# Kernel optimization log

Hardware: AMD Instinct MI355X
Metric: run time of the kernel (lower is better)

The kernel has to match this reference:

```python
import jax, jax.numpy as jnp
import numpy as np

N = 100000        # nodes
E = 3200000       # edges
IN = 256          # in_feats
H = 8             # num_heads
O = 64            # out_feats
F = 64            # edge_feats
T = 8             # num_etypes

def setup_inputs() -> dict:
    key = jax.random.key(0)
    ks = jax.random.split(key, 10)
    return {
        "feat": jax.random.normal(ks[0], (N, IN), jnp.float32) * 0.1,
        "etype": jax.random.randint(ks[1], (E,), 0, T, jnp.int32),
        "src": jax.random.randint(ks[2], (E,), 0, N, jnp.int32),
        "dst": jax.random.randint(ks[3], (E,), 0, N, jnp.int32),
        "W_fc": jax.random.normal(ks[4], (IN, H * O), jnp.float32) * (1.0 / np.sqrt(IN)),
        "edge_emb": jax.random.normal(ks[5], (T, F), jnp.float32),
        "W_e": jax.random.normal(ks[6], (F, H * F), jnp.float32) * (1.0 / np.sqrt(F)),
        "attn_l": jax.random.normal(ks[7], (H, O), jnp.float32) * 0.1,
        "attn_r": jax.random.normal(ks[8], (H, O), jnp.float32) * 0.1,
        "attn_e": jax.random.normal(ks[9], (H, F), jnp.float32) * 0.1,
    }

def reference(feat, etype, src, dst, W_fc, edge_emb, W_e, attn_l, attn_r, attn_e):
    n = feat.shape[0]
    # node projection + per-head attention logits
    h = (feat @ W_fc).reshape(n, H, O)                      # [N,H,O]
    el = jnp.einsum('nho,ho->nh', h, attn_l)                # [N,H]
    er = jnp.einsum('nho,ho->nh', h, attn_r)                # [N,H]
    # edge-type embedding -> projection -> logit (project the tiny table once, then gather)
    emb_proj = (edge_emb @ W_e).reshape(T, H, F)            # [T,H,F]
    ee = jnp.einsum('thf,hf->th', emb_proj, attn_e)[etype]  # [E,H]
    # u_add_v + edge bias, then ReLU (module's "leaky_relu" is nn.ReLU())
    e = jax.nn.relu(el[src] + er[dst] + ee)                 # [E,H]
    # segment softmax grouped by destination node
    m = jax.ops.segment_max(e, dst, num_segments=n)         # [N,H]
    ex = jnp.exp(e - m[dst])                                # [E,H]
    s = jax.ops.segment_sum(ex, dst, num_segments=n)        # [N,H]
    return ex / s[dst]                                      # [E,H]
```

## Files before the change

### kernel.cpp

```cpp
#include <hip/hip_runtime.h>
#include <math.h>

#define NN 100000
#define NE 3200000
#define INF_ 256
#define NH 8
#define OF 64
#define EF 64
#define NT 8

#define BSH 7
#define BNODES 128
#define NB 782
#define CAPB 4608
#define SPLIT 2
#define CHUNK 2304
#define EPB 4096

static constexpr size_t WS_AT      = 0;
static constexpr size_t WS_EE      = 4096;
static constexpr size_t WS_EL      = 4160;
static constexpr size_t WS_ERS     = WS_EL + (size_t)NN * 8;
static constexpr size_t WS_CCNT    = WS_ERS + (size_t)NN * 16;
static constexpr size_t WS_PART    = WS_CCNT + NB + 2;
static constexpr size_t WS_PARTIAL = WS_PART + (size_t)NB * CAPB;

__global__ __launch_bounds__(256) void k_prep_A(const float* __restrict__ W_fc,
                                                const float* __restrict__ attn_l,
                                                const float* __restrict__ attn_r,
                                                float* __restrict__ At,
                                                unsigned* __restrict__ ccnt) {
    int t = blockIdx.x * 256 + threadIdx.x;
    if (t < NB) ccnt[t] = 0u;
    int c = t >> 8;
    int i = t & 255;
    int h = c & 7;
    const float* attn = (c < 8) ? attn_l : attn_r;
    const float* wrow = W_fc + (size_t)i * (NH * OF) + h * OF;
    const float* arow = attn + h * OF;
    float acc = 0.f;
#pragma unroll 8
    for (int o = 0; o < OF; ++o) acc += wrow[o] * arow[o];
    At[c * INF_ + i] = acc;
}

__global__ __launch_bounds__(512) void k_prep_ee(const float* __restrict__ edge_emb,
                                                 const float* __restrict__ W_e,
                                                 const float* __restrict__ attn_e,
                                                 float* __restrict__ ee_tab) {
    __shared__ float B[EF][NH];
    int t = threadIdx.x;
    int g = t >> 3, h = t & 7;
    const float* wrow = W_e + (size_t)g * (NH * EF) + h * EF;
    const float* arow = attn_e + h * EF;
    float acc = 0.f;
#pragma unroll 8
    for (int f = 0; f < EF; ++f) acc += wrow[f] * arow[f];
    B[g][h] = acc;
    __syncthreads();
    if (t < NT * NH) {
        int tt = t >> 3, hh = t & 7;
        float a = 0.f;
#pragma unroll 8
        for (int g2 = 0; g2 < EF; ++g2) a += edge_emb[tt * EF + g2] * B[g2][hh];
        ee_tab[tt * NH + hh] = a;
    }
}

__global__ __launch_bounds__(256) void k_node(const float* __restrict__ feat,
                                              const float* __restrict__ At,
                                              float* __restrict__ el,
                                              float* __restrict__ ers) {
    int n = blockIdx.x * 256 + threadIdx.x;
    if (n >= NN) return;
    const float4* f4 = (const float4*)(feat + (size_t)n * INF_);
    const float4* A4 = (const float4*)At;
    float acc[16];
#pragma unroll
    for (int c = 0; c < 16; ++c) acc[c] = 0.f;
    for (int iq = 0; iq < INF_ / 4; ++iq) {
        float4 f = f4[iq];
#pragma unroll
        for (int c = 0; c < 16; ++c) {
            float4 a = A4[c * 64 + iq];
            acc[c] += f.x * a.x + f.y * a.y + f.z * a.z + f.w * a.w;
        }
    }
    float4* e4 = (float4*)(el + (size_t)n * 8);
    e4[0] = make_float4(acc[0], acc[1], acc[2], acc[3]);
    e4[1] = make_float4(acc[4], acc[5], acc[6], acc[7]);
    float4* r4 = (float4*)(ers + (size_t)n * 16);
    r4[0] = make_float4(acc[8], acc[9], acc[10], acc[11]);
    r4[1] = make_float4(acc[12], acc[13], acc[14], acc[15]);
}

__global__ __launch_bounds__(256) void k_partition(const int* __restrict__ src,
                                                   const int* __restrict__ dst,
                                                   const int* __restrict__ etype,
                                                   unsigned* __restrict__ ccnt,
                                                   unsigned* __restrict__ part) {
    __shared__ unsigned hist[NB];
    __shared__ unsigned cursor[NB];
    int tid = threadIdx.x;
    size_t base = (size_t)blockIdx.x * EPB;
    unsigned long long rc[16];
    for (int i = tid; i < NB; i += 256) hist[i] = 0u;
    __syncthreads();
#pragma unroll
    for (int k = 0; k < 16; ++k) {
        size_t j = base + (size_t)k * 256 + tid;
        if (j < NE) {
            int dj = dst[j];
            rc[k] = (unsigned long long)(unsigned)src[j]
                  | ((unsigned long long)(unsigned)etype[j] << 17)
                  | ((unsigned long long)(unsigned)dj << 20);
            atomicAdd(&hist[dj >> BSH], 1u);
        } else rc[k] = ~0ull;
    }
    __syncthreads();
    for (int i = tid; i < NB; i += 256) {
        unsigned h = hist[i];
        cursor[i] = h ? atomicAdd(ccnt + i, h) : 0u;
    }
    __syncthreads();
#pragma unroll
    for (int k = 0; k < 16; ++k) {
        if (rc[k] == ~0ull) continue;
        int dj = (int)(rc[k] >> 20);
        int b = dj >> BSH;
        unsigned pos = atomicAdd(&cursor[b], 1u);
        if (pos < CAPB)
            part[(size_t)b * CAPB + pos] =
                (unsigned)(rc[k] & 0xFFFFFull) | ((unsigned)(dj & (BNODES - 1)) << 20);
    }
}

__global__ __launch_bounds__(256) void k_bucket_sum(const unsigned* __restrict__ part,
                                                    const unsigned* __restrict__ ccnt,
                                                    const float* __restrict__ el,
                                                    const float* __restrict__ ers,
                                                    const float* __restrict__ ee_tab,
                                                    float* __restrict__ partial) {
    __shared__ float sbin[BNODES * 9];
    __shared__ float er_l[BNODES * 9];
    __shared__ float ee_l[NT * NH];
    int bs = blockIdx.x;
    int b = bs >> 1, c = bs & 1;
    int tid = threadIdx.x;
    int e_sub = tid >> 3, h = tid & 7;
    int n0 = b << BSH;
    int nn = NN - n0; if (nn > BNODES) nn = BNODES;

    for (int i = tid; i < BNODES * 9; i += 256) sbin[i] = 0.f;
    if (tid < NT * NH) ee_l[tid] = ee_tab[tid];
    for (int i = tid; i < nn * NH; i += 256) {
        int nl = i >> 3, hh = i & 7;
        er_l[nl * 9 + hh] = ers[(size_t)(n0 + nl) * 16 + hh];
    }
    __syncthreads();

    unsigned cnt = ccnt[b]; if (cnt > CAPB) cnt = CAPB;
    unsigned hi = (unsigned)(c + 1) * CHUNK; if (hi > cnt) hi = cnt;
    const unsigned* pp = part + (size_t)b * CAPB;
    for (unsigned e = (unsigned)c * CHUNK + e_sub; e < hi; e += 32) {
        unsigned rec = pp[e];
        int sj = (int)(rec & 0x1FFFFu);
        int et = (int)((rec >> 17) & 7u);
        int dl = (int)((rec >> 20) & (BNODES - 1));
        float v = el[(size_t)sj * 8 + h] + er_l[dl * 9 + h] + ee_l[et * NH + h];
        atomicAdd(&sbin[dl * 9 + h], expf(fmaxf(v, 0.f)));
    }
    __syncthreads();
    float* po = partial + ((size_t)b * SPLIT + c) * (BNODES * NH);
    for (int i = tid; i < nn * NH; i += 256)
        po[i] = sbin[(i >> 3) * 9 + (i & 7)];
}

__global__ __launch_bounds__(256) void k_reduce(const float* __restrict__ partial,
                                                float* __restrict__ ers) {
    int t = blockIdx.x * 256 + threadIdx.x;
    if (t >= NN * NH) return;
    int n = t >> 3, h = t & 7;
    int b = n >> BSH, nl = n & (BNODES - 1);
    const float* pa = partial + (size_t)b * SPLIT * (BNODES * NH);
    ers[(size_t)n * 16 + 8 + h] = pa[nl * NH + h] + pa[BNODES * NH + nl * NH + h];
}

__global__ __launch_bounds__(256) void k_edge_out(const int* __restrict__ src,
                                                  const int* __restrict__ dst,
                                                  const int* __restrict__ etype,
                                                  const float* __restrict__ el,
                                                  const float* __restrict__ ers,
                                                  const float* __restrict__ ee_tab,
                                                  float* __restrict__ out) {
    int j = blockIdx.x * 256 + threadIdx.x;
    if (j >= NE) return;
    int sj = src[j], dj = dst[j], tj = etype[j];
    const float4* el4 = (const float4*)(el + (size_t)sj * 8);
    const float4* E   = (const float4*)(ers + (size_t)dj * 16);
    const float4* ee4 = (const float4*)(ee_tab + tj * NH);
    float4 l0 = el4[0], l1 = el4[1];
    float4 r0 = E[0], r1 = E[1];
    float4 s0 = E[2], s1 = E[3];
    float4 e0 = ee4[0], e1 = ee4[1];
    float4 o0, o1;
    o0.x = expf(fmaxf(l0.x + r0.x + e0.x, 0.f)) / s0.x;
    o0.y = expf(fmaxf(l0.y + r0.y + e0.y, 0.f)) / s0.y;
    o0.z = expf(fmaxf(l0.z + r0.z + e0.z, 0.f)) / s0.z;
    o0.w = expf(fmaxf(l0.w + r0.w + e0.w, 0.f)) / s0.w;
    o1.x = expf(fmaxf(l1.x + r1.x + e1.x, 0.f)) / s1.x;
    o1.y = expf(fmaxf(l1.y + r1.y + e1.y, 0.f)) / s1.y;
    o1.z = expf(fmaxf(l1.z + r1.z + e1.z, 0.f)) / s1.z;
    o1.w = expf(fmaxf(l1.w + r1.w + e1.w, 0.f)) / s1.w;
    float4* o4 = (float4*)(out + (size_t)j * NH);
    o4[0] = o0;
    o4[1] = o1;
}

extern "C" void kernel_launch(void* const* d_in, const int* in_sizes, int n_in,
                              void* d_out, int out_size, void* d_ws, size_t ws_size,
                              hipStream_t stream) {
    const float* feat     = (const float*)d_in[0];
    const int*   etype    = (const int*)d_in[1];
    const int*   src      = (const int*)d_in[2];
    const int*   dst      = (const int*)d_in[3];
    const float* W_fc     = (const float*)d_in[4];
    const float* edge_emb = (const float*)d_in[5];
    const float* W_e      = (const float*)d_in[6];
    const float* attn_l   = (const float*)d_in[7];
    const float* attn_r   = (const float*)d_in[8];
    const float* attn_e   = (const float*)d_in[9];

    float*    ws      = (float*)d_ws;
    float*    At      = ws + WS_AT;
    float*    ee_tab  = ws + WS_EE;
    float*    el      = ws + WS_EL;
    float*    ers     = ws + WS_ERS;
    unsigned* ccnt    = (unsigned*)(ws + WS_CCNT);
    unsigned* part    = (unsigned*)(ws + WS_PART);
    float*    partial = ws + WS_PARTIAL;
    float*    out     = (float*)d_out;

    hipLaunchKernelGGL(k_prep_A, dim3(16), dim3(256), 0, stream, W_fc, attn_l, attn_r, At, ccnt);
    hipLaunchKernelGGL(k_prep_ee, dim3(1), dim3(512), 0, stream, edge_emb, W_e, attn_e, ee_tab);
    hipLaunchKernelGGL(k_node, dim3((NN + 255) / 256), dim3(256), 0, stream, feat, At, el, ers);
    hipLaunchKernelGGL(k_partition, dim3((NE + EPB - 1) / EPB), dim3(256), 0, stream,
                       src, dst, etype, ccnt, part);
    hipLaunchKernelGGL(k_bucket_sum, dim3(NB * SPLIT), dim3(256), 0, stream,
                       part, ccnt, el, ers, ee_tab, partial);
    hipLaunchKernelGGL(k_reduce, dim3((NN * NH + 255) / 256), dim3(256), 0, stream,
                       partial, ers);
    hipLaunchKernelGGL(k_edge_out, dim3((NE + 255) / 256), dim3(256), 0, stream,
                       src, dst, etype, el, ers, ee_tab, out);
}
```

Baseline: 557.3 us.

## Fuse bucket partial reduction into atomics, split buckets four ways, unroll edge loop

The bucket-sum kernel now splits each destination bucket across four blocks instead of two, and unrolls the edge loop by four so the gathered source-logit loads are issued together. Each block atomically adds its shared-memory sums straight into the per-node sum slots. Those slots are zeroed in the node kernel, so the separate reduce kernel and the partial buffer are gone. This saves one launch and a round trip through global memory, and the extra blocks add parallelism. The cost is global float atomics, which make the summation order nondeterministic, and each bucket's shared-memory setup is now repeated across more blocks.

```diff
diff --git a/kernel.cpp b/kernel.cpp
--- a/kernel.cpp
+++ b/kernel.cpp
@@ -13,8 +13,8 @@
 #define BNODES 128
 #define NB 782
 #define CAPB 4608
-#define SPLIT 2
-#define CHUNK 2304
+#define SPLIT 4
+#define CHUNK 1152
 #define EPB 4096
 
 static constexpr size_t WS_AT      = 0;
@@ -23,7 +23,6 @@
 static constexpr size_t WS_ERS     = WS_EL + (size_t)NN * 8;
 static constexpr size_t WS_CCNT    = WS_ERS + (size_t)NN * 16;
 static constexpr size_t WS_PART    = WS_CCNT + NB + 2;
-static constexpr size_t WS_PARTIAL = WS_PART + (size_t)NB * CAPB;
 
 __global__ __launch_bounds__(256) void k_prep_A(const float* __restrict__ W_fc,
                                                 const float* __restrict__ attn_l,
@@ -92,6 +91,8 @@
     float4* r4 = (float4*)(ers + (size_t)n * 16);
     r4[0] = make_float4(acc[8], acc[9], acc[10], acc[11]);
     r4[1] = make_float4(acc[12], acc[13], acc[14], acc[15]);
+    r4[2] = make_float4(0.f, 0.f, 0.f, 0.f);
+    r4[3] = make_float4(0.f, 0.f, 0.f, 0.f);
 }
 
 __global__ __launch_bounds__(256) void k_partition(const int* __restrict__ src,
@@ -140,12 +141,12 @@
                                                     const float* __restrict__ el,
                                                     const float* __restrict__ ers,
                                                     const float* __restrict__ ee_tab,
-                                                    float* __restrict__ partial) {
+                                                    float* __restrict__ ers_out) {
     __shared__ float sbin[BNODES * 9];
     __shared__ float er_l[BNODES * 9];
     __shared__ float ee_l[NT * NH];
     int bs = blockIdx.x;
-    int b = bs >> 1, c = bs & 1;
+    int b = bs >> 2, c = bs & 3;
     int tid = threadIdx.x;
     int e_sub = tid >> 3, h = tid & 7;
     int n0 = b << BSH;
@@ -160,9 +161,41 @@
     __syncthreads();
 
     unsigned cnt = ccnt[b]; if (cnt > CAPB) cnt = CAPB;
-    unsigned hi = (unsigned)(c + 1) * CHUNK; if (hi > cnt) hi = cnt;
+    unsigned lo = (unsigned)c * CHUNK;
+    unsigned hi = lo + CHUNK; if (hi > cnt) hi = cnt;
     const unsigned* pp = part + (size_t)b * CAPB;
-    for (unsigned e = (unsigned)c * CHUNK + e_sub; e < hi; e += 32) {
+    unsigned e = lo + (unsigned)e_sub;
+    for (; e + 96 < hi; e += 128) {
+        unsigned r0 = pp[e];
+        unsigned r1 = pp[e + 32];
+        unsigned r2 = pp[e + 64];
+        unsigned r3 = pp[e + 96];
+        float l0 = el[(size_t)(r0 & 0x1FFFFu) * 8 + h];
+        float l1 = el[(size_t)(r1 & 0x1FFFFu) * 8 + h];
+        float l2 = el[(size_t)(r2 & 0x1FFFFu) * 8 + h];
+        float l3 = el[(size_t)(r3 & 0x1FFFFu) * 8 + h];
+        {
+            int et = (int)((r0 >> 17) & 7u), dl = (int)((r0 >> 20) & (BNODES - 1));
+            float v = l0 + er_l[dl * 9 + h] + ee_l[et * NH + h];
+            atomicAdd(&sbin[dl * 9 + h], expf(fmaxf(v, 0.f)));
+        }
+        {
+            int et = (int)((r1 >> 17) & 7u), dl = (int)((r1 >> 20) & (BNODES - 1));
+            float v = l1 + er_l[dl * 9 + h] + ee_l[et * NH + h];
+            atomicAdd(&sbin[dl * 9 + h], expf(fmaxf(v, 0.f)));
+        }
+        {
+            int et = (int)((r2 >> 17) & 7u), dl = (int)((r2 >> 20) & (BNODES - 1));
+            float v = l2 + er_l[dl * 9 + h] + ee_l[et * NH + h];
+            atomicAdd(&sbin[dl * 9 + h], expf(fmaxf(v, 0.f)));
+        }
+        {
+            int et = (int)((r3 >> 17) & 7u), dl = (int)((r3 >> 20) & (BNODES - 1));
+            float v = l3 + er_l[dl * 9 + h] + ee_l[et * NH + h];
+            atomicAdd(&sbin[dl * 9 + h], expf(fmaxf(v, 0.f)));
+        }
+    }
+    for (; e < hi; e += 32) {
         unsigned rec = pp[e];
         int sj = (int)(rec & 0x1FFFFu);
         int et = (int)((rec >> 17) & 7u);
@@ -171,19 +204,10 @@
         atomicAdd(&sbin[dl * 9 + h], expf(fmaxf(v, 0.f)));
     }
     __syncthreads();
-    float* po = partial + ((size_t)b * SPLIT + c) * (BNODES * NH);
-    for (int i = tid; i < nn * NH; i += 256)
-        po[i] = sbin[(i >> 3) * 9 + (i & 7)];
-}
-
-__global__ __launch_bounds__(256) void k_reduce(const float* __restrict__ partial,
-                                                float* __restrict__ ers) {
-    int t = blockIdx.x * 256 + threadIdx.x;
-    if (t >= NN * NH) return;
-    int n = t >> 3, h = t & 7;
-    int b = n >> BSH, nl = n & (BNODES - 1);
-    const float* pa = partial + (size_t)b * SPLIT * (BNODES * NH);
-    ers[(size_t)n * 16 + 8 + h] = pa[nl * NH + h] + pa[BNODES * NH + nl * NH + h];
+    for (int i = tid; i < nn * NH; i += 256) {
+        int nl = i >> 3, hh = i & 7;
+        atomicAdd(&ers_out[(size_t)(n0 + nl) * 16 + 8 + hh], sbin[nl * 9 + hh]);
+    }
 }
 
 __global__ __launch_bounds__(256) void k_edge_out(const int* __restrict__ src,
@@ -238,7 +262,6 @@
     float*    ers     = ws + WS_ERS;
     unsigned* ccnt    = (unsigned*)(ws + WS_CCNT);
     unsigned* part    = (unsigned*)(ws + WS_PART);
-    float*    partial = ws + WS_PARTIAL;
     float*    out     = (float*)d_out;
 
     hipLaunchKernelGGL(k_prep_A, dim3(16), dim3(256), 0, stream, W_fc, attn_l, attn_r, At, ccnt);
@@ -247,9 +270,7 @@
     hipLaunchKernelGGL(k_partition, dim3((NE + EPB - 1) / EPB), dim3(256), 0, stream,
                        src, dst, etype, ccnt, part);
     hipLaunchKernelGGL(k_bucket_sum, dim3(NB * SPLIT), dim3(256), 0, stream,
-                       part, ccnt, el, ers, ee_tab, partial);
-    hipLaunchKernelGGL(k_reduce, dim3((NN * NH + 255) / 256), dim3(256), 0, stream,
-                       partial, ers);
+                       part, ccnt, el, ers, ee_tab, ers);
     hipLaunchKernelGGL(k_edge_out, dim3((NE + 255) / 256), dim3(256), 0, stream,
                        src, dst, etype, el, ers, ee_tab, out);
 }
```

After: 541.2 us. 2.9% less time.
